# Optimization experiments

Hardware: AMD Instinct MI355X
Metric: run time of the kernel (lower is better)

Reference implementation:

```python
import math
import jax, jax.numpy as jnp
import numpy as np

B, C, E = 8, 2048, 1024

def setup_inputs() -> dict:
    key = jax.random.key(0)
    ks = jax.random.split(key, 7)
    s_e = 1.0 / math.sqrt(E)
    s_c = 1.0 / math.sqrt(C)
    return {
        'x': jax.random.normal(ks[0], (B, C, E), dtype=jnp.float32),
        'fc_w': jax.random.normal(ks[1], (E, E), dtype=jnp.float32) * s_e,
        'fc_b': jax.random.normal(ks[2], (E,), dtype=jnp.float32) * s_e,
        'alt_fc_w': jax.random.normal(ks[3], (C, C), dtype=jnp.float32) * s_c,
        'alt_fc_b': jax.random.normal(ks[4], (C,), dtype=jnp.float32) * s_c,
        'vfc_w': jax.random.normal(ks[5], (E, E), dtype=jnp.float32) * s_e,
        'vfc_b': jax.random.normal(ks[6], (E,), dtype=jnp.float32) * s_e,
    }

def reference(x, fc_w, fc_b, alt_fc_w, alt_fc_b, vfc_w, vfc_b):
    # y = fc(x): [b,c,e]
    y = jnp.einsum('bce,fe->bcf', x, fc_w) + fc_b
    # yx = alt_fc(x^T): [b,e,c] -> Linear over context dim -> [b,e,k]
    xx = jnp.swapaxes(x, 1, 2)                    # [b,e,c]
    yx = jnp.einsum('bec,kc->bek', xx, alt_fc_w) + alt_fc_b
    # attention scores: [b,c,k]
    attn = jnp.einsum('bce,bek->bck', y, yx)
    scale = 1.0 / math.sqrt(attn.shape[-1])
    attn = jax.nn.softmax(attn * scale, axis=-1)
    # values
    vx = jnp.einsum('bke,fe->bkf', x, vfc_w) + vfc_b
    out = jnp.einsum('bck,bke->bce', attn, vx)
    # post_feed=None -> return y only
    return out
```

## Files before the change

kernel.cpp:

```cpp
#include <hip/hip_runtime.h>
#include <stdint.h>

#define Bb 8
#define Cc 2048
#define Ee 1024

typedef unsigned short u16;
typedef __attribute__((ext_vector_type(8))) short short8;
typedef __attribute__((ext_vector_type(4))) float f32x4;

__device__ __forceinline__ u16 f2bf(float f){
    unsigned u = __builtin_bit_cast(unsigned, f);
    return (u16)((u + 0x7fffu + ((u >> 16) & 1u)) >> 16);
}
__device__ __forceinline__ float bf2f(u16 h){
    return __builtin_bit_cast(float, ((unsigned)h) << 16);
}
__device__ __forceinline__ void gld16(const void* g, void* l){
    __builtin_amdgcn_global_load_lds(
        (const __attribute__((address_space(1))) unsigned int*)g,
        (__attribute__((address_space(3))) unsigned int*)l,
        16, 0, 0);
}
#define MFMA(a,b,c) __builtin_amdgcn_mfma_f32_16x16x32_bf16((a),(b),(c),0,0,0)
#define SBAR()  __builtin_amdgcn_s_barrier()
#define SCHED0() __builtin_amdgcn_sched_barrier(0)
#define LGKM0() asm volatile("s_waitcnt lgkmcnt(0)" ::: "memory")

__global__ __launch_bounds__(256) void k_cast(const float* __restrict__ s,
                                              u16* __restrict__ d, long n4){
    long i = (long)blockIdx.x * 256 + threadIdx.x;
    const long stride = (long)gridDim.x * 256;
    for (; i < n4; i += stride){
        float4 f = ((const float4*)s)[i];
        ushort4 o = make_ushort4(f2bf(f.x), f2bf(f.y), f2bf(f.z), f2bf(f.w));
        ((ushort4*)d)[i] = o;
    }
}

__global__ __launch_bounds__(256) void k_cast_transpose(const float* __restrict__ src,
                                                        u16* __restrict__ dst){
    __shared__ float tile[32][33];
    const int b = blockIdx.z;
    src += (long)b * Cc * Ee;
    dst += (long)b * Cc * Ee;
    const int c0 = blockIdx.x * 32;
    const int r0 = blockIdx.y * 32;
    const int tx = threadIdx.x & 31;
    const int ty = threadIdx.x >> 5;
    #pragma unroll
    for (int p = 0; p < 4; ++p)
        tile[ty + p*8][tx] = src[(long)(r0 + ty + p*8) * Ee + c0 + tx];
    __syncthreads();
    #pragma unroll
    for (int p = 0; p < 4; ++p)
        dst[(long)(c0 + ty + p*8) * Cc + r0 + tx] = f2bf(tile[tx][ty + p*8]);
}

template<int BIAS_MODE, int OUT_F32>
__global__ __launch_bounds__(512, 2)
void k_gemm256(const u16* __restrict__ A, const u16* __restrict__ Bm,
               void* __restrict__ Cout, const float* __restrict__ bias,
               int N, int K, long sA, long sB, long sC, float scale)
{
    __shared__ __attribute__((aligned(16))) char smem[131072];
    const int bz = blockIdx.z;
    A  += (long)bz * sA;
    Bm += (long)bz * sB;
    u16*   Cm = (u16*)Cout + (OUT_F32 ? 0 : (long)bz * sC);
    float* Cf = (float*)Cout + (OUT_F32 ? (long)bz * sC : 0);

    const int tid  = threadIdx.x;
    const int lane = tid & 63;
    const int wave = tid >> 6;
    const int wr = wave >> 2;
    const int wc = wave & 3;
    const int tileM = blockIdx.x * 256;
    const int tileN = blockIdx.y * 256;

    const int srow   = tid >> 3;
    const int schunk = (tid & 7) ^ (srow & 7);
    const u16* Ag = A  + (long)(tileM + srow) * K + schunk * 8;
    const u16* Bg = Bm + (long)(tileN + srow) * K + schunk * 8;
    const long uK = (long)64 * K;
    const int  ldst = tid * 16;

    const int lrow = lane & 15;
    const int lk   = lane >> 4;
    const int sw   = lrow & 7;
    const int cs0  = ((0 + lk) ^ sw) * 16;
    const int cs1  = ((4 + lk) ^ sw) * 16;
    const int arow0 = (wr*128 + lrow) * 128;
    const int brow0 = 32768 + (wc*64 + lrow) * 128;

    f32x4 acc[8][4];
    #pragma unroll
    for (int m = 0; m < 8; ++m)
        #pragma unroll
        for (int n = 0; n < 4; ++n)
            acc[m][n] = (f32x4){0.f,0.f,0.f,0.f};

    char* sm = smem;
    #pragma unroll
    for (int u = 0; u < 4; ++u) gld16(Bg + u*uK, sm + 32768 + u*8192 + ldst);
    #pragma unroll
    for (int u = 0; u < 4; ++u) gld16(Ag + u*uK, sm + u*8192 + ldst);
    __syncthreads();

    const int NT = K >> 6;
    short8 aF[4][2], bF[2][2];

    for (int t = 0; t < NT; ++t){
        const bool pref = (t + 1) < NT;
        char* cbuf = sm + ((t & 1) << 16);
        char* nbuf = sm + (((t + 1) & 1) << 16);
        const u16* Agt = Ag + (t + 1) * 64;
        const u16* Bgt = Bg + (t + 1) * 64;

        #pragma unroll
        for (int m = 0; m < 4; ++m){
            aF[m][0] = *(const short8*)(cbuf + arow0 + m*2048 + cs0);
            aF[m][1] = *(const short8*)(cbuf + arow0 + m*2048 + cs1);
        }
        #pragma unroll
        for (int n = 0; n < 2; ++n){
            bF[n][0] = *(const short8*)(cbuf + brow0 + n*2048 + cs0);
            bF[n][1] = *(const short8*)(cbuf + brow0 + n*2048 + cs1);
        }
        if (pref){ gld16(Bgt + 0*uK, nbuf + 32768 + 0*8192 + ldst);
                   gld16(Bgt + 1*uK, nbuf + 32768 + 1*8192 + ldst); }
        SCHED0(); SBAR(); LGKM0(); SCHED0();
        __builtin_amdgcn_s_setprio(1);
        #pragma unroll
        for (int m = 0; m < 4; ++m)
            #pragma unroll
            for (int n = 0; n < 2; ++n){
                acc[m][n] = MFMA(aF[m][0], bF[n][0], acc[m][n]);
                acc[m][n] = MFMA(aF[m][1], bF[n][1], acc[m][n]);
            }
        __builtin_amdgcn_s_setprio(0);
        SBAR(); SCHED0();

        #pragma unroll
        for (int n = 0; n < 2; ++n){
            bF[n][0] = *(const short8*)(cbuf + brow0 + (n+2)*2048 + cs0);
            bF[n][1] = *(const short8*)(cbuf + brow0 + (n+2)*2048 + cs1);
        }
        if (pref){ gld16(Bgt + 2*uK, nbuf + 32768 + 2*8192 + ldst);
                   gld16(Bgt + 3*uK, nbuf + 32768 + 3*8192 + ldst); }
        SCHED0(); SBAR(); LGKM0(); SCHED0();
        __builtin_amdgcn_s_setprio(1);
        #pragma unroll
        for (int m = 0; m < 4; ++m)
            #pragma unroll
            for (int n = 0; n < 2; ++n){
                acc[m][n+2] = MFMA(aF[m][0], bF[n][0], acc[m][n+2]);
                acc[m][n+2] = MFMA(aF[m][1], bF[n][1], acc[m][n+2]);
            }
        __builtin_amdgcn_s_setprio(0);
        if (pref){ asm volatile("s_waitcnt vmcnt(4)" ::: "memory"); }
        else     { asm volatile("s_waitcnt vmcnt(0)" ::: "memory"); }
        SBAR(); SCHED0();

        #pragma unroll
        for (int m = 0; m < 4; ++m){
            aF[m][0] = *(const short8*)(cbuf + arow0 + (m+4)*2048 + cs0);
            aF[m][1] = *(const short8*)(cbuf + arow0 + (m+4)*2048 + cs1);
        }
        if (pref){ gld16(Agt + 0*uK, nbuf + 0*8192 + ldst);
                   gld16(Agt + 2*uK, nbuf + 2*8192 + ldst); }
        SCHED0(); SBAR(); LGKM0(); SCHED0();
        __builtin_amdgcn_s_setprio(1);
        #pragma unroll
        for (int m = 0; m < 4; ++m)
            #pragma unroll
            for (int n = 0; n < 2; ++n){
                acc[m+4][n+2] = MFMA(aF[m][0], bF[n][0], acc[m+4][n+2]);
                acc[m+4][n+2] = MFMA(aF[m][1], bF[n][1], acc[m+4][n+2]);
            }
        __builtin_amdgcn_s_setprio(0);
        SBAR(); SCHED0();

        #pragma unroll
        for (int n = 0; n < 2; ++n){
            bF[n][0] = *(const short8*)(cbuf + brow0 + n*2048 + cs0);
            bF[n][1] = *(const short8*)(cbuf + brow0 + n*2048 + cs1);
        }
        if (pref){ gld16(Agt + 1*uK, nbuf + 1*8192 + ldst);
                   gld16(Agt + 3*uK, nbuf + 3*8192 + ldst); }
        SCHED0(); SBAR(); LGKM0(); SCHED0();
        __builtin_amdgcn_s_setprio(1);
        #pragma unroll
        for (int m = 0; m < 4; ++m)
            #pragma unroll
            for (int n = 0; n < 2; ++n){
                acc[m+4][n] = MFMA(aF[m][0], bF[n][0], acc[m+4][n]);
                acc[m+4][n] = MFMA(aF[m][1], bF[n][1], acc[m+4][n]);
            }
        __builtin_amdgcn_s_setprio(0);
        asm volatile("s_waitcnt vmcnt(2)" ::: "memory");
        SBAR(); SCHED0();
    }

    const int r0base = tileM + wr*128 + lk*4;
    const int cbase  = tileN + wc*64 + lrow;
    #pragma unroll
    for (int m = 0; m < 8; ++m){
        const int r0 = r0base + m*16;
        #pragma unroll
        for (int n = 0; n < 4; ++n){
            const int c = cbase + n*16;
            f32x4 v = acc[m][n];
            #pragma unroll
            for (int j = 0; j < 4; ++j){
                float val = v[j] * scale;
                if (BIAS_MODE == 1) val += bias[c];
                if (BIAS_MODE == 2) val += bias[r0 + j];
                if (OUT_F32) Cf[(long)(r0 + j) * N + c] = val;
                else         Cm[(long)(r0 + j) * N + c] = f2bf(val);
            }
        }
    }
}

__global__ __launch_bounds__(256) void k_softmax(u16* __restrict__ P){
    u16* p = P + (long)blockIdx.x * Cc;
    const int tid = threadIdx.x;
    short8 raw = *(const short8*)(p + tid * 8);
    float v[8];
    float mx = -3.0e38f;
    #pragma unroll
    for (int i = 0; i < 8; ++i){ v[i] = bf2f((u16)raw[i]); mx = fmaxf(mx, v[i]); }
    #pragma unroll
    for (int o = 32; o > 0; o >>= 1) mx = fmaxf(mx, __shfl_xor(mx, o));
    __shared__ float redm[4];
    if ((tid & 63) == 0) redm[tid >> 6] = mx;
    __syncthreads();
    mx = fmaxf(fmaxf(redm[0], redm[1]), fmaxf(redm[2], redm[3]));
    float s = 0.f;
    #pragma unroll
    for (int i = 0; i < 8; ++i){ v[i] = __expf(v[i] - mx); s += v[i]; }
    #pragma unroll
    for (int o = 32; o > 0; o >>= 1) s += __shfl_xor(s, o);
    __shared__ float reds[4];
    if ((tid & 63) == 0) reds[tid >> 6] = s;
    __syncthreads();
    s = reds[0] + reds[1] + reds[2] + reds[3];
    const float inv = 1.f / s;
    short8 o8;
    #pragma unroll
    for (int i = 0; i < 8; ++i) o8[i] = (short)f2bf(v[i] * inv);
    *(short8*)(p + tid * 8) = o8;
}

static inline int cast_grid(long n4){
    long g = (n4 + 255) / 256;
    return (int)(g > 2048 ? 2048 : g);
}

extern "C" void kernel_launch(void* const* d_in, const int* in_sizes, int n_in,
                              void* d_out, int out_size, void* d_ws, size_t ws_size,
                              hipStream_t stream)
{
    const float* x     = (const float*)d_in[0];
    const float* fc_w  = (const float*)d_in[1];
    const float* fc_b  = (const float*)d_in[2];
    const float* altw  = (const float*)d_in[3];
    const float* altb  = (const float*)d_in[4];
    const float* vfc_w = (const float*)d_in[5];
    const float* vfc_b = (const float*)d_in[6];
    float* out = (float*)d_out;

    char* ws = (char*)d_ws;
    const size_t nBCE = (size_t)Bb * Cc * Ee;
    u16* xb   = (u16*)(ws);
    u16* xbT  = (u16*)(ws + 2 * nBCE);
    u16* P    = (u16*)(ws);
    u16* y    = (u16*)(ws + 4 * nBCE);
    u16* z    = (u16*)(ws + 6 * nBCE);
    u16* vxT  = (u16*)(ws + 8 * nBCE);
    u16* fcwb = (u16*)(ws + 10 * nBCE);
    u16* vfwb = fcwb + (size_t)Ee * Ee;
    u16* awb  = vfwb + (size_t)Ee * Ee;

    k_cast<<<cast_grid((long)nBCE / 4), 256, 0, stream>>>(x, xb, (long)nBCE / 4);
    k_cast<<<cast_grid((long)Ee * Ee / 4), 256, 0, stream>>>(fc_w, fcwb, (long)Ee * Ee / 4);
    k_cast<<<cast_grid((long)Ee * Ee / 4), 256, 0, stream>>>(vfc_w, vfwb, (long)Ee * Ee / 4);
    k_cast<<<cast_grid((long)Cc * Cc / 4), 256, 0, stream>>>(altw, awb, (long)Cc * Cc / 4);
    k_cast_transpose<<<dim3(Ee / 32, Cc / 32, Bb), 256, 0, stream>>>(x, xbT);

    const long sBCE = (long)Cc * Ee;
    const long sBCC = (long)Cc * Cc;
    dim3 blk(512);

    k_gemm256<1, 0><<<dim3(Cc/256, Ee/256, Bb), blk, 0, stream>>>(
        xb, fcwb, y, fc_b, Ee, Ee, sBCE, 0, sBCE, 1.f);

    k_gemm256<2, 0><<<dim3(Ee/256, Cc/256, Bb), blk, 0, stream>>>(
        vfwb, xb, vxT, vfc_b, Cc, Ee, 0, sBCE, sBCE, 1.f);

    k_gemm256<2, 0><<<dim3(Cc/256, Ee/256, Bb), blk, 0, stream>>>(
        awb, xbT, z, altb, Ee, Cc, 0, sBCE, sBCE, 1.f);

    k_gemm256<0, 0><<<dim3(Cc/256, Cc/256, Bb), blk, 0, stream>>>(
        y, z, P, nullptr, Cc, Ee, sBCE, sBCE, sBCC, 0.022097086912079608f);

    k_softmax<<<Bb * Cc, 256, 0, stream>>>(P);

    k_gemm256<0, 1><<<dim3(Cc/256, Ee/256, Bb), blk, 0, stream>>>(
        P, vxT, out, nullptr, Ee, Cc, sBCC, sBCE, sBCE, 1.f);
}
```

Baseline: 368.3 us.

## Fuse x cast with transpose, swizzle GEMM block order, reorder MFMA K-phases

```diff
diff --git a/kernel.cpp b/kernel.cpp
--- a/kernel.cpp
+++ b/kernel.cpp
@@ -26,6 +26,8 @@
 #define SBAR()  __builtin_amdgcn_s_barrier()
 #define SCHED0() __builtin_amdgcn_sched_barrier(0)
 #define LGKM0() asm volatile("s_waitcnt lgkmcnt(0)" ::: "memory")
+#define VMCNT2() asm volatile("s_waitcnt vmcnt(2)" ::: "memory")
+#define VMCNT0() asm volatile("s_waitcnt vmcnt(0)" ::: "memory")
 
 __global__ __launch_bounds__(256) void k_cast(const float* __restrict__ s,
                                               u16* __restrict__ d, long n4){
@@ -38,23 +40,28 @@
     }
 }
 
-__global__ __launch_bounds__(256) void k_cast_transpose(const float* __restrict__ src,
-                                                        u16* __restrict__ dst){
+__global__ __launch_bounds__(256) void k_cast_xt(const float* __restrict__ src,
+                                                 u16* __restrict__ xb,
+                                                 u16* __restrict__ xbT){
     __shared__ float tile[32][33];
     const int b = blockIdx.z;
     src += (long)b * Cc * Ee;
-    dst += (long)b * Cc * Ee;
+    xb  += (long)b * Cc * Ee;
+    xbT += (long)b * Cc * Ee;
     const int c0 = blockIdx.x * 32;
     const int r0 = blockIdx.y * 32;
     const int tx = threadIdx.x & 31;
     const int ty = threadIdx.x >> 5;
     #pragma unroll
+    for (int p = 0; p < 4; ++p){
+        float v = src[(long)(r0 + ty + p*8) * Ee + c0 + tx];
+        tile[ty + p*8][tx] = v;
+        xb[(long)(r0 + ty + p*8) * Ee + c0 + tx] = f2bf(v);
+    }
+    __syncthreads();
+    #pragma unroll
     for (int p = 0; p < 4; ++p)
-        tile[ty + p*8][tx] = src[(long)(r0 + ty + p*8) * Ee + c0 + tx];
-    __syncthreads();
-    #pragma unroll
-    for (int p = 0; p < 4; ++p)
-        dst[(long)(c0 + ty + p*8) * Cc + r0 + tx] = f2bf(tile[tx][ty + p*8]);
+        xbT[(long)(c0 + ty + p*8) * Cc + r0 + tx] = f2bf(tile[tx][ty + p*8]);
 }
 
 template<int BIAS_MODE, int OUT_F32>
@@ -64,7 +71,16 @@
                int N, int K, long sA, long sB, long sC, float scale)
 {
     __shared__ __attribute__((aligned(16))) char smem[131072];
-    const int bz = blockIdx.z;
+
+    const int gx = gridDim.x, gy = gridDim.y;
+    const int nwg = gx * gy * gridDim.z;
+    const int lin = blockIdx.x + gx * (blockIdx.y + gy * blockIdx.z);
+    const int swz = (lin & 7) * (nwg >> 3) + (lin >> 3);
+    const int bx = swz % gx;
+    const int tmp = swz / gx;
+    const int by = tmp % gy;
+    const int bz = tmp / gy;
+
     A  += (long)bz * sA;
     Bm += (long)bz * sB;
     u16*   Cm = (u16*)Cout + (OUT_F32 ? 0 : (long)bz * sC);
@@ -75,8 +91,8 @@
     const int wave = tid >> 6;
     const int wr = wave >> 2;
     const int wc = wave & 3;
-    const int tileM = blockIdx.x * 256;
-    const int tileN = blockIdx.y * 256;
+    const int tileM = bx * 256;
+    const int tileN = by * 256;
 
     const int srow   = tid >> 3;
     const int schunk = (tid & 7) ^ (srow & 7);
@@ -108,25 +124,34 @@
     __syncthreads();
 
     const int NT = K >> 6;
-    short8 aF[4][2], bF[2][2];
+    short8 aF[4], bF[4];
 
     for (int t = 0; t < NT; ++t){
         const bool pref = (t + 1) < NT;
         char* cbuf = sm + ((t & 1) << 16);
         char* nbuf = sm + (((t + 1) & 1) << 16);
-        const u16* Agt = Ag + (t + 1) * 64;
-        const u16* Bgt = Bg + (t + 1) * 64;
-
-        #pragma unroll
-        for (int m = 0; m < 4; ++m){
-            aF[m][0] = *(const short8*)(cbuf + arow0 + m*2048 + cs0);
-            aF[m][1] = *(const short8*)(cbuf + arow0 + m*2048 + cs1);
-        }
-        #pragma unroll
-        for (int n = 0; n < 2; ++n){
-            bF[n][0] = *(const short8*)(cbuf + brow0 + n*2048 + cs0);
-            bF[n][1] = *(const short8*)(cbuf + brow0 + n*2048 + cs1);
-        }
+        const u16* Agt = Ag + (long)(t + 1) * 64;
+        const u16* Bgt = Bg + (long)(t + 1) * 64;
+
+        #pragma unroll
+        for (int m = 0; m < 4; ++m) aF[m] = *(const short8*)(cbuf + arow0 + m*2048 + cs0);
+        #pragma unroll
+        for (int n = 0; n < 4; ++n) bF[n] = *(const short8*)(cbuf + brow0 + n*2048 + cs0);
+        if (pref){ gld16(Agt + 0*uK, nbuf + 0*8192 + ldst);
+                   gld16(Agt + 2*uK, nbuf + 2*8192 + ldst); }
+        SCHED0(); SBAR(); LGKM0(); SCHED0();
+        __builtin_amdgcn_s_setprio(1);
+        #pragma unroll
+        for (int m = 0; m < 4; ++m)
+            #pragma unroll
+            for (int n = 0; n < 4; ++n)
+                acc[m][n] = MFMA(aF[m], bF[n], acc[m][n]);
+        __builtin_amdgcn_s_setprio(0);
+        if (pref){ VMCNT2(); } else { VMCNT0(); }
+        SBAR(); SCHED0();
+
+        #pragma unroll
+        for (int m = 0; m < 4; ++m) aF[m] = *(const short8*)(cbuf + arow0 + (m+4)*2048 + cs0);
         if (pref){ gld16(Bgt + 0*uK, nbuf + 32768 + 0*8192 + ldst);
                    gld16(Bgt + 1*uK, nbuf + 32768 + 1*8192 + ldst); }
         SCHED0(); SBAR(); LGKM0(); SCHED0();
@@ -134,18 +159,15 @@
         #pragma unroll
         for (int m = 0; m < 4; ++m)
             #pragma unroll
-            for (int n = 0; n < 2; ++n){
-                acc[m][n] = MFMA(aF[m][0], bF[n][0], acc[m][n]);
-                acc[m][n] = MFMA(aF[m][1], bF[n][1], acc[m][n]);
-            }
+            for (int n = 0; n < 4; ++n)
+                acc[m+4][n] = MFMA(aF[m], bF[n], acc[m+4][n]);
         __builtin_amdgcn_s_setprio(0);
         SBAR(); SCHED0();
 
         #pragma unroll
-        for (int n = 0; n < 2; ++n){
-            bF[n][0] = *(const short8*)(cbuf + brow0 + (n+2)*2048 + cs0);
-            bF[n][1] = *(const short8*)(cbuf + brow0 + (n+2)*2048 + cs1);
-        }
+        for (int m = 0; m < 4; ++m) aF[m] = *(const short8*)(cbuf + arow0 + m*2048 + cs1);
+        #pragma unroll
+        for (int n = 0; n < 4; ++n) bF[n] = *(const short8*)(cbuf + brow0 + n*2048 + cs1);
         if (pref){ gld16(Bgt + 2*uK, nbuf + 32768 + 2*8192 + ldst);
                    gld16(Bgt + 3*uK, nbuf + 32768 + 3*8192 + ldst); }
         SCHED0(); SBAR(); LGKM0(); SCHED0();
@@ -153,39 +175,13 @@
         #pragma unroll
         for (int m = 0; m < 4; ++m)
             #pragma unroll
-            for (int n = 0; n < 2; ++n){
-                acc[m][n+2] = MFMA(aF[m][0], bF[n][0], acc[m][n+2]);
-                acc[m][n+2] = MFMA(aF[m][1], bF[n][1], acc[m][n+2]);
-            }
-        __builtin_amdgcn_s_setprio(0);
-        if (pref){ asm volatile("s_waitcnt vmcnt(4)" ::: "memory"); }
-        else     { asm volatile("s_waitcnt vmcnt(0)" ::: "memory"); }
-        SBAR(); SCHED0();
-
-        #pragma unroll
-        for (int m = 0; m < 4; ++m){
-            aF[m][0] = *(const short8*)(cbuf + arow0 + (m+4)*2048 + cs0);
-            aF[m][1] = *(const short8*)(cbuf + arow0 + (m+4)*2048 + cs1);
-        }
-        if (pref){ gld16(Agt + 0*uK, nbuf + 0*8192 + ldst);
-                   gld16(Agt + 2*uK, nbuf + 2*8192 + ldst); }
-        SCHED0(); SBAR(); LGKM0(); SCHED0();
-        __builtin_amdgcn_s_setprio(1);
-        #pragma unroll
-        for (int m = 0; m < 4; ++m)
-            #pragma unroll
-            for (int n = 0; n < 2; ++n){
-                acc[m+4][n+2] = MFMA(aF[m][0], bF[n][0], acc[m+4][n+2]);
-                acc[m+4][n+2] = MFMA(aF[m][1], bF[n][1], acc[m+4][n+2]);
-            }
+            for (int n = 0; n < 4; ++n)
+                acc[m][n] = MFMA(aF[m], bF[n], acc[m][n]);
         __builtin_amdgcn_s_setprio(0);
         SBAR(); SCHED0();
 
         #pragma unroll
-        for (int n = 0; n < 2; ++n){
-            bF[n][0] = *(const short8*)(cbuf + brow0 + n*2048 + cs0);
-            bF[n][1] = *(const short8*)(cbuf + brow0 + n*2048 + cs1);
-        }
+        for (int m = 0; m < 4; ++m) aF[m] = *(const short8*)(cbuf + arow0 + (m+4)*2048 + cs1);
         if (pref){ gld16(Agt + 1*uK, nbuf + 1*8192 + ldst);
                    gld16(Agt + 3*uK, nbuf + 3*8192 + ldst); }
         SCHED0(); SBAR(); LGKM0(); SCHED0();
@@ -193,12 +189,10 @@
         #pragma unroll
         for (int m = 0; m < 4; ++m)
             #pragma unroll
-            for (int n = 0; n < 2; ++n){
-                acc[m+4][n] = MFMA(aF[m][0], bF[n][0], acc[m+4][n]);
-                acc[m+4][n] = MFMA(aF[m][1], bF[n][1], acc[m+4][n]);
-            }
+            for (int n = 0; n < 4; ++n)
+                acc[m+4][n] = MFMA(aF[m], bF[n], acc[m+4][n]);
         __builtin_amdgcn_s_setprio(0);
-        asm volatile("s_waitcnt vmcnt(2)" ::: "memory");
+        if (pref){ VMCNT2(); }
         SBAR(); SCHED0();
     }
 
@@ -283,11 +277,10 @@
     u16* vfwb = fcwb + (size_t)Ee * Ee;
     u16* awb  = vfwb + (size_t)Ee * Ee;
 
-    k_cast<<<cast_grid((long)nBCE / 4), 256, 0, stream>>>(x, xb, (long)nBCE / 4);
+    k_cast_xt<<<dim3(Ee / 32, Cc / 32, Bb), 256, 0, stream>>>(x, xb, xbT);
     k_cast<<<cast_grid((long)Ee * Ee / 4), 256, 0, stream>>>(fc_w, fcwb, (long)Ee * Ee / 4);
     k_cast<<<cast_grid((long)Ee * Ee / 4), 256, 0, stream>>>(vfc_w, vfwb, (long)Ee * Ee / 4);
     k_cast<<<cast_grid((long)Cc * Cc / 4), 256, 0, stream>>>(altw, awb, (long)Cc * Cc / 4);
-    k_cast_transpose<<<dim3(Ee / 32, Cc / 32, Bb), 256, 0, stream>>>(x, xbT);
 
     const long sBCE = (long)Cc * Ee;
     const long sBCC = (long)Cc * Cc;
```

Measured after the change: 353.5 us. 1.04x faster.
